# Performance work log

Measured on AMD Instinct MI355X. Metric: run time of the kernel, lower is better.

The kernel has to match this reference:

```python
import jax, jax.numpy as jnp
import numpy as np

B, T, IN, H = 512, 512, 1, 64


def _lstm_dir(x, w_ih, w_hh, b_ih, b_hh, reverse):
    """Single-direction LSTM over x:[B,T,D]. PyTorch gate order i,f,g,o."""
    # Precompute input contribution for all timesteps (one big GEMM).
    xg = jnp.einsum('btd,gd->btg', x, w_ih) + (b_ih + b_hh)  # [B,T,4H]
    if reverse:
        xg = xg[:, ::-1]
    Hh = w_hh.shape[1]
    w_hh_t = w_hh.T  # [H,4H]

    def step(carry, g_t):
        h, c = carry
        g = g_t + h @ w_hh_t  # [B,4H]
        i, f, gc, o = jnp.split(g, 4, axis=-1)
        c = jax.nn.sigmoid(f) * c + jax.nn.sigmoid(i) * jnp.tanh(gc)
        h = jax.nn.sigmoid(o) * jnp.tanh(c)
        return (h, c), h

    b = x.shape[0]
    init = (jnp.zeros((b, Hh), x.dtype), jnp.zeros((b, Hh), x.dtype))
    _, hs = jax.lax.scan(step, init, jnp.swapaxes(xg, 0, 1))  # hs:[T,B,H]
    hs = jnp.swapaxes(hs, 0, 1)  # [B,T,H]
    return hs[:, ::-1] if reverse else hs


def _bilstm_layer(x, wf, rf, bf, bf2, wr, rr, br, br2):
    fwd = _lstm_dir(x, wf, rf, bf, bf2, reverse=False)
    bwd = _lstm_dir(x, wr, rr, br, br2, reverse=True)
    return jnp.concatenate([fwd, bwd], axis=-1)  # [B,T,2H]


def setup_inputs() -> dict:
    key = jax.random.key(0)
    ks = jax.random.split(key, 20)
    s = 1.0 / np.sqrt(H)
    u = lambda k, shape: jax.random.uniform(k, shape, jnp.float32, -s, s)
    inp = {'x': jax.random.normal(ks[0], (B, T, IN), jnp.float32)}
    # layer 0 (input dim IN), layer 1 (input dim 2H), fwd and reverse dirs
    inp['w_ih_l0'] = u(ks[1], (4 * H, IN)); inp['w_hh_l0'] = u(ks[2], (4 * H, H))
    inp['b_ih_l0'] = u(ks[3], (4 * H,));   inp['b_hh_l0'] = u(ks[4], (4 * H,))
    inp['w_ih_l0r'] = u(ks[5], (4 * H, IN)); inp['w_hh_l0r'] = u(ks[6], (4 * H, H))
    inp['b_ih_l0r'] = u(ks[7], (4 * H,));    inp['b_hh_l0r'] = u(ks[8], (4 * H,))
    inp['w_ih_l1'] = u(ks[9], (4 * H, 2 * H)); inp['w_hh_l1'] = u(ks[10], (4 * H, H))
    inp['b_ih_l1'] = u(ks[11], (4 * H,));      inp['b_hh_l1'] = u(ks[12], (4 * H,))
    inp['w_ih_l1r'] = u(ks[13], (4 * H, 2 * H)); inp['w_hh_l1r'] = u(ks[14], (4 * H, H))
    inp['b_ih_l1r'] = u(ks[15], (4 * H,));       inp['b_hh_l1r'] = u(ks[16], (4 * H,))
    inp['fc_w'] = u(ks[17], (1, 2 * H)); inp['fc_b'] = u(ks[18], (1,))
    return inp


def reference(x, w_ih_l0, w_hh_l0, b_ih_l0, b_hh_l0,
              w_ih_l0r, w_hh_l0r, b_ih_l0r, b_hh_l0r,
              w_ih_l1, w_hh_l1, b_ih_l1, b_hh_l1,
              w_ih_l1r, w_hh_l1r, b_ih_l1r, b_hh_l1r,
              fc_w, fc_b):
    h0 = _bilstm_layer(x, w_ih_l0, w_hh_l0, b_ih_l0, b_hh_l0,
                       w_ih_l0r, w_hh_l0r, b_ih_l0r, b_hh_l0r)
    h1 = _bilstm_layer(h0, w_ih_l1, w_hh_l1, b_ih_l1, b_hh_l1,
                       w_ih_l1r, w_hh_l1r, b_ih_l1r, b_hh_l1r)
    last = h1[:, -1, :]  # [B,2H]
    return last @ fc_w.T + fc_b  # [B,1]
```

## Files before the change

### kernel.cpp

```cpp
#include <hip/hip_runtime.h>
#include <cstddef>
#include <cstdint>

#define Tn 512
#define Bn 512
#define Hn 64

__device__ __forceinline__ float rlane(float v, int lane) {
    return __uint_as_float((unsigned)__builtin_amdgcn_readlane((int)__float_as_uint(v), lane));
}
__device__ __forceinline__ float sigm(float x) { return 1.0f / (1.0f + __expf(-x)); }
__device__ __forceinline__ float tanhf_(float x) { return 1.0f - 2.0f / (1.0f + __expf(2.0f * x)); }

__global__ __launch_bounds__(64, 1) void k_lstm_l0(
    const float* __restrict__ x,
    const float* __restrict__ wih_f, const float* __restrict__ whh_f,
    const float* __restrict__ bih_f, const float* __restrict__ bhh_f,
    const float* __restrict__ wih_r, const float* __restrict__ whh_r,
    const float* __restrict__ bih_r, const float* __restrict__ bhh_r,
    float* __restrict__ h0)
{
    const int task = blockIdx.x;
    const int b = task >> 1;
    const int dir = task & 1;
    const int j = threadIdx.x;

    const float* __restrict__ wih = dir ? wih_r : wih_f;
    const float* __restrict__ whh = dir ? whh_r : whh_f;
    const float* __restrict__ bih = dir ? bih_r : bih_f;
    const float* __restrict__ bhh = dir ? bhh_r : bhh_f;

    __shared__ float xs[Tn];
    #pragma unroll
    for (int i = 0; i < Tn / 64; ++i) xs[i * 64 + j] = x[b * Tn + i * 64 + j];
    __syncthreads();

    float w[4][64];
    float wx[4], bias[4];
    #pragma unroll
    for (int g = 0; g < 4; ++g) {
        const int r = g * 64 + j;
        wx[g] = wih[r];
        bias[g] = bih[r] + bhh[r];
        #pragma unroll
        for (int k4 = 0; k4 < 16; ++k4) {
            const float4 v = *reinterpret_cast<const float4*>(&whh[r * 64 + k4 * 4]);
            w[g][k4 * 4 + 0] = v.x; w[g][k4 * 4 + 1] = v.y;
            w[g][k4 * 4 + 2] = v.z; w[g][k4 * 4 + 3] = v.w;
        }
    }

    float h = 0.0f, c = 0.0f;
    float* __restrict__ outp = h0 + (size_t)b * Tn * 128 + dir * 64 + j;

    for (int s = 0; s < Tn; ++s) {
        const int t = dir ? (Tn - 1 - s) : s;
        const float xt = xs[t];
        float a0 = fmaf(xt, wx[0], bias[0]);
        float a1 = fmaf(xt, wx[1], bias[1]);
        float a2 = fmaf(xt, wx[2], bias[2]);
        float a3 = fmaf(xt, wx[3], bias[3]);
        #pragma unroll
        for (int k = 0; k < 64; ++k) {
            const float hk = rlane(h, k);
            a0 = fmaf(hk, w[0][k], a0);
            a1 = fmaf(hk, w[1][k], a1);
            a2 = fmaf(hk, w[2][k], a2);
            a3 = fmaf(hk, w[3][k], a3);
        }
        c = sigm(a1) * c + sigm(a0) * tanhf_(a2);
        h = sigm(a3) * tanhf_(c);
        outp[(size_t)t * 128] = h;
    }
}

__global__ __launch_bounds__(256, 2) void k_lstm_l1f(
    const float* __restrict__ h0,
    const float* __restrict__ wih, const float* __restrict__ whh,
    const float* __restrict__ bih, const float* __restrict__ bhh,
    float* __restrict__ h1last)
{
    const int b = blockIdx.x;
    const int tid = threadIdx.x;
    const int wv = tid >> 6;
    const int j = tid & 63;

    float bias[4];
    #pragma unroll
    for (int g = 0; g < 4; ++g) {
        const int r = g * 64 + j;
        bias[g] = bih[r] + bhh[r];
    }

    float wt[4][48];
    if (wv == 0) {
        #pragma unroll
        for (int g = 0; g < 4; ++g) {
            const int r = g * 64 + j;
            #pragma unroll
            for (int kk = 0; kk < 48; ++kk) wt[g][kk] = wih[r * 128 + kk];
        }
    } else if (wv == 1) {
        #pragma unroll
        for (int g = 0; g < 4; ++g) {
            const int r = g * 64 + j;
            #pragma unroll
            for (int kk = 0; kk < 48; ++kk) wt[g][kk] = wih[r * 128 + 48 + kk];
        }
    } else if (wv == 2) {
        #pragma unroll
        for (int g = 0; g < 4; ++g) {
            const int r = g * 64 + j;
            #pragma unroll
            for (int kk = 0; kk < 48; ++kk)
                wt[g][kk] = (kk < 32) ? wih[r * 128 + 96 + kk] : whh[r * 64 + (kk - 32)];
        }
    } else {
        #pragma unroll
        for (int g = 0; g < 4; ++g) {
            const int r = g * 64 + j;
            #pragma unroll
            for (int kk = 0; kk < 48; ++kk) wt[g][kk] = whh[r * 64 + 16 + kk];
        }
    }

    const float* __restrict__ xrow = h0 + (size_t)b * Tn * 128;
    float x1a = xrow[j];
    float x1b = xrow[64 + j];
    float h = 0.0f, c = 0.0f;

    __shared__ float part[2][4][64][4];

    for (int t = 0; t < Tn; ++t) {
        float nx1a = 0.0f, nx1b = 0.0f;
        if (t + 1 < Tn) {
            nx1a = xrow[(t + 1) * 128 + j];
            nx1b = xrow[(t + 1) * 128 + 64 + j];
        }
        float a0 = 0.0f, a1 = 0.0f, a2 = 0.0f, a3 = 0.0f;
        if (wv == 0) {
            #pragma unroll
            for (int kk = 0; kk < 48; ++kk) {
                const float v = rlane(x1a, kk);
                a0 = fmaf(v, wt[0][kk], a0); a1 = fmaf(v, wt[1][kk], a1);
                a2 = fmaf(v, wt[2][kk], a2); a3 = fmaf(v, wt[3][kk], a3);
            }
        } else if (wv == 1) {
            #pragma unroll
            for (int kk = 0; kk < 48; ++kk) {
                const float v = (kk < 16) ? rlane(x1a, 48 + kk) : rlane(x1b, kk - 16);
                a0 = fmaf(v, wt[0][kk], a0); a1 = fmaf(v, wt[1][kk], a1);
                a2 = fmaf(v, wt[2][kk], a2); a3 = fmaf(v, wt[3][kk], a3);
            }
        } else if (wv == 2) {
            #pragma unroll
            for (int kk = 0; kk < 48; ++kk) {
                const float v = (kk < 32) ? rlane(x1b, 32 + kk) : rlane(h, kk - 32);
                a0 = fmaf(v, wt[0][kk], a0); a1 = fmaf(v, wt[1][kk], a1);
                a2 = fmaf(v, wt[2][kk], a2); a3 = fmaf(v, wt[3][kk], a3);
            }
        } else {
            #pragma unroll
            for (int kk = 0; kk < 48; ++kk) {
                const float v = rlane(h, 16 + kk);
                a0 = fmaf(v, wt[0][kk], a0); a1 = fmaf(v, wt[1][kk], a1);
                a2 = fmaf(v, wt[2][kk], a2); a3 = fmaf(v, wt[3][kk], a3);
            }
        }
        *reinterpret_cast<float4*>(&part[t & 1][wv][j][0]) = make_float4(a0, a1, a2, a3);
        __syncthreads();
        const float4 p0 = *reinterpret_cast<const float4*>(&part[t & 1][0][j][0]);
        const float4 p1 = *reinterpret_cast<const float4*>(&part[t & 1][1][j][0]);
        const float4 p2 = *reinterpret_cast<const float4*>(&part[t & 1][2][j][0]);
        const float4 p3 = *reinterpret_cast<const float4*>(&part[t & 1][3][j][0]);
        const float gi = bias[0] + p0.x + p1.x + p2.x + p3.x;
        const float gf = bias[1] + p0.y + p1.y + p2.y + p3.y;
        const float gg = bias[2] + p0.z + p1.z + p2.z + p3.z;
        const float go = bias[3] + p0.w + p1.w + p2.w + p3.w;
        c = sigm(gf) * c + sigm(gi) * tanhf_(gg);
        h = sigm(go) * tanhf_(c);
        x1a = nx1a; x1b = nx1b;
    }
    if (tid < 64) h1last[(size_t)b * 64 + j] = h;
}

__global__ __launch_bounds__(64, 1) void k_l1r_fc(
    const float* __restrict__ h0,
    const float* __restrict__ wihr,
    const float* __restrict__ bihr, const float* __restrict__ bhhr,
    const float* __restrict__ h1last,
    const float* __restrict__ fcw, const float* __restrict__ fcb,
    float* __restrict__ out)
{
    const int b = blockIdx.x;
    const int j = threadIdx.x;
    const float* __restrict__ xrow = h0 + ((size_t)b * Tn + (Tn - 1)) * 128;
    const float x1a = xrow[j];
    const float x1b = xrow[64 + j];
    float acc[4];
    #pragma unroll
    for (int g = 0; g < 4; ++g) {
        const int r = g * 64 + j;
        float a = bihr[r] + bhhr[r];
        const float* __restrict__ wr = wihr + (size_t)r * 128;
        #pragma unroll
        for (int d4 = 0; d4 < 16; ++d4) {
            const float4 w4 = *reinterpret_cast<const float4*>(&wr[d4 * 4]);
            a = fmaf(rlane(x1a, d4 * 4 + 0), w4.x, a);
            a = fmaf(rlane(x1a, d4 * 4 + 1), w4.y, a);
            a = fmaf(rlane(x1a, d4 * 4 + 2), w4.z, a);
            a = fmaf(rlane(x1a, d4 * 4 + 3), w4.w, a);
        }
        #pragma unroll
        for (int d4 = 0; d4 < 16; ++d4) {
            const float4 w4 = *reinterpret_cast<const float4*>(&wr[64 + d4 * 4]);
            a = fmaf(rlane(x1b, d4 * 4 + 0), w4.x, a);
            a = fmaf(rlane(x1b, d4 * 4 + 1), w4.y, a);
            a = fmaf(rlane(x1b, d4 * 4 + 2), w4.z, a);
            a = fmaf(rlane(x1b, d4 * 4 + 3), w4.w, a);
        }
        acc[g] = a;
    }
    const float cr = sigm(acc[0]) * tanhf_(acc[2]);
    const float hr = sigm(acc[3]) * tanhf_(cr);
    float v = h1last[(size_t)b * 64 + j] * fcw[j] + hr * fcw[64 + j];
    #pragma unroll
    for (int off = 32; off > 0; off >>= 1) v += __shfl_xor(v, off, 64);
    if (j == 0) out[b] = v + fcb[0];
}

extern "C" void kernel_launch(void* const* d_in, const int* in_sizes, int n_in,
                              void* d_out, int out_size, void* d_ws, size_t ws_size,
                              hipStream_t stream)
{
    const float* x       = (const float*)d_in[0];
    const float* wih_l0  = (const float*)d_in[1];
    const float* whh_l0  = (const float*)d_in[2];
    const float* bih_l0  = (const float*)d_in[3];
    const float* bhh_l0  = (const float*)d_in[4];
    const float* wih_l0r = (const float*)d_in[5];
    const float* whh_l0r = (const float*)d_in[6];
    const float* bih_l0r = (const float*)d_in[7];
    const float* bhh_l0r = (const float*)d_in[8];
    const float* wih_l1  = (const float*)d_in[9];
    const float* whh_l1  = (const float*)d_in[10];
    const float* bih_l1  = (const float*)d_in[11];
    const float* bhh_l1  = (const float*)d_in[12];
    const float* wih_l1r = (const float*)d_in[13];
    const float* whh_l1r = (const float*)d_in[14];
    const float* bih_l1r = (const float*)d_in[15];
    const float* bhh_l1r = (const float*)d_in[16];
    const float* fcw     = (const float*)d_in[17];
    const float* fcb     = (const float*)d_in[18];
    (void)whh_l1r; (void)in_sizes; (void)n_in; (void)out_size;

    float* h0     = (float*)d_ws;
    float* h1last = h0 + (size_t)Bn * Tn * 128;
    (void)ws_size;

    k_lstm_l0<<<dim3(Bn * 2), dim3(64), 0, stream>>>(
        x, wih_l0, whh_l0, bih_l0, bhh_l0,
        wih_l0r, whh_l0r, bih_l0r, bhh_l0r, h0);
    k_lstm_l1f<<<dim3(Bn), dim3(256), 0, stream>>>(
        h0, wih_l1, whh_l1, bih_l1, bhh_l1, h1last);
    k_l1r_fc<<<dim3(Bn), dim3(64), 0, stream>>>(
        h0, wih_l1r, bih_l1r, bhh_l1r, h1last, fcw, fcb, (float*)d_out);
}
```

Baseline: 1.207 ms.

## Split LSTM recurrence K-dimension across more waves in both layer kernels

Layer 0 now runs both directions of a batch row in one 256-thread block, with each direction's 64-wide hidden dot product split across two waves whose partial gate sums are combined through shared memory. Layer 1 forward uses six waves of 32 K-columns each, so every wave does a uniform 32-step readlane/FMA loop instead of four waves doing 48. Two waves redundantly apply the gate nonlinearities and feed h back as their next input. This shortens the serial per-step dependency chain and lowers register pressure, at the cost of an extra barrier per step in layer 0 and more waves competing for each CU.

```diff
diff --git a/kernel.cpp b/kernel.cpp
--- a/kernel.cpp
+++ b/kernel.cpp
@@ -4,7 +4,6 @@
 
 #define Tn 512
 #define Bn 512
-#define Hn 64
 
 __device__ __forceinline__ float rlane(float v, int lane) {
     return __uint_as_float((unsigned)__builtin_amdgcn_readlane((int)__float_as_uint(v), lane));
@@ -12,7 +11,9 @@
 __device__ __forceinline__ float sigm(float x) { return 1.0f / (1.0f + __expf(-x)); }
 __device__ __forceinline__ float tanhf_(float x) { return 1.0f - 2.0f / (1.0f + __expf(2.0f * x)); }
 
-__global__ __launch_bounds__(64, 1) void k_lstm_l0(
+#define BAR_LGKM() asm volatile("s_waitcnt lgkmcnt(0)\n\ts_barrier" ::: "memory")
+
+__global__ __launch_bounds__(256, 2) void k_lstm_l0(
     const float* __restrict__ x,
     const float* __restrict__ wih_f, const float* __restrict__ whh_f,
     const float* __restrict__ bih_f, const float* __restrict__ bhh_f,
@@ -20,168 +21,148 @@
     const float* __restrict__ bih_r, const float* __restrict__ bhh_r,
     float* __restrict__ h0)
 {
-    const int task = blockIdx.x;
-    const int b = task >> 1;
-    const int dir = task & 1;
-    const int j = threadIdx.x;
+    const int b   = blockIdx.x;
+    const int tid = threadIdx.x;
+    const int wv  = tid >> 6;
+    const int dir = wv >> 1;
+    const int kh  = wv & 1;
+    const int j   = tid & 63;
+    const int klo = kh * 32;
 
     const float* __restrict__ wih = dir ? wih_r : wih_f;
     const float* __restrict__ whh = dir ? whh_r : whh_f;
     const float* __restrict__ bih = dir ? bih_r : bih_f;
     const float* __restrict__ bhh = dir ? bhh_r : bhh_f;
 
-    __shared__ float xs[Tn];
-    #pragma unroll
-    for (int i = 0; i < Tn / 64; ++i) xs[i * 64 + j] = x[b * Tn + i * 64 + j];
-    __syncthreads();
-
-    float w[4][64];
+    __shared__ float  xs[Tn];
+    __shared__ float4 part[2][4][64];
+
+    #pragma unroll
+    for (int i = 0; i < Tn / 256; ++i) xs[i * 256 + tid] = x[b * Tn + i * 256 + tid];
+
+    float wt[4][32];
     float wx[4], bias[4];
     #pragma unroll
     for (int g = 0; g < 4; ++g) {
         const int r = g * 64 + j;
-        wx[g] = wih[r];
+        wx[g]   = wih[r];
         bias[g] = bih[r] + bhh[r];
-        #pragma unroll
-        for (int k4 = 0; k4 < 16; ++k4) {
-            const float4 v = *reinterpret_cast<const float4*>(&whh[r * 64 + k4 * 4]);
-            w[g][k4 * 4 + 0] = v.x; w[g][k4 * 4 + 1] = v.y;
-            w[g][k4 * 4 + 2] = v.z; w[g][k4 * 4 + 3] = v.w;
-        }
-    }
+        const float* __restrict__ ws = whh + (size_t)r * 64 + klo;
+        #pragma unroll
+        for (int k4 = 0; k4 < 8; ++k4) {
+            const float4 w4 = *reinterpret_cast<const float4*>(ws + k4 * 4);
+            wt[g][k4 * 4 + 0] = w4.x; wt[g][k4 * 4 + 1] = w4.y;
+            wt[g][k4 * 4 + 2] = w4.z; wt[g][k4 * 4 + 3] = w4.w;
+        }
+    }
+    __syncthreads();
 
     float h = 0.0f, c = 0.0f;
     float* __restrict__ outp = h0 + (size_t)b * Tn * 128 + dir * 64 + j;
 
     for (int s = 0; s < Tn; ++s) {
-        const int t = dir ? (Tn - 1 - s) : s;
+        const int t  = dir ? (Tn - 1 - s) : s;
+        const int bf = s & 1;
         const float xt = xs[t];
-        float a0 = fmaf(xt, wx[0], bias[0]);
-        float a1 = fmaf(xt, wx[1], bias[1]);
-        float a2 = fmaf(xt, wx[2], bias[2]);
-        float a3 = fmaf(xt, wx[3], bias[3]);
-        #pragma unroll
-        for (int k = 0; k < 64; ++k) {
-            const float hk = rlane(h, k);
-            a0 = fmaf(hk, w[0][k], a0);
-            a1 = fmaf(hk, w[1][k], a1);
-            a2 = fmaf(hk, w[2][k], a2);
-            a3 = fmaf(hk, w[3][k], a3);
-        }
-        c = sigm(a1) * c + sigm(a0) * tanhf_(a2);
-        h = sigm(a3) * tanhf_(c);
-        outp[(size_t)t * 128] = h;
-    }
-}
-
-__global__ __launch_bounds__(256, 2) void k_lstm_l1f(
+
+        float a0 = 0.0f, a1 = 0.0f, a2 = 0.0f, a3 = 0.0f;
+        #pragma unroll
+        for (int kk = 0; kk < 32; ++kk) {
+            const float hk = rlane(h, klo + kk);
+            a0 = fmaf(hk, wt[0][kk], a0);
+            a1 = fmaf(hk, wt[1][kk], a1);
+            a2 = fmaf(hk, wt[2][kk], a2);
+            a3 = fmaf(hk, wt[3][kk], a3);
+        }
+        part[bf][wv][j] = make_float4(a0, a1, a2, a3);
+        BAR_LGKM();
+        const float4 pA = part[bf][dir * 2 + 0][j];
+        const float4 pB = part[bf][dir * 2 + 1][j];
+        const float gi = fmaf(xt, wx[0], bias[0]) + pA.x + pB.x;
+        const float gf = fmaf(xt, wx[1], bias[1]) + pA.y + pB.y;
+        const float gg = fmaf(xt, wx[2], bias[2]) + pA.z + pB.z;
+        const float go = fmaf(xt, wx[3], bias[3]) + pA.w + pB.w;
+        c = sigm(gf) * c + sigm(gi) * tanhf_(gg);
+        h = sigm(go) * tanhf_(c);
+        if (kh == 0) outp[(size_t)t * 128] = h;
+    }
+}
+
+__global__ __launch_bounds__(384, 3) void k_lstm_l1f(
     const float* __restrict__ h0,
     const float* __restrict__ wih, const float* __restrict__ whh,
     const float* __restrict__ bih, const float* __restrict__ bhh,
     float* __restrict__ h1last)
 {
-    const int b = blockIdx.x;
+    const int b   = blockIdx.x;
     const int tid = threadIdx.x;
-    const int wv = tid >> 6;
-    const int j = tid & 63;
-
+    const int wv  = tid / 64;
+    const int j   = tid & 63;
+    const int lb  = (wv & 1) * 32;
+    const int kbase = wv * 32;
+
+    __shared__ float4 part[2][6][64];
+
+    float wt[4][32];
     float bias[4];
     #pragma unroll
     for (int g = 0; g < 4; ++g) {
         const int r = g * 64 + j;
         bias[g] = bih[r] + bhh[r];
-    }
-
-    float wt[4][48];
-    if (wv == 0) {
-        #pragma unroll
-        for (int g = 0; g < 4; ++g) {
-            const int r = g * 64 + j;
-            #pragma unroll
-            for (int kk = 0; kk < 48; ++kk) wt[g][kk] = wih[r * 128 + kk];
-        }
-    } else if (wv == 1) {
-        #pragma unroll
-        for (int g = 0; g < 4; ++g) {
-            const int r = g * 64 + j;
-            #pragma unroll
-            for (int kk = 0; kk < 48; ++kk) wt[g][kk] = wih[r * 128 + 48 + kk];
-        }
-    } else if (wv == 2) {
-        #pragma unroll
-        for (int g = 0; g < 4; ++g) {
-            const int r = g * 64 + j;
-            #pragma unroll
-            for (int kk = 0; kk < 48; ++kk)
-                wt[g][kk] = (kk < 32) ? wih[r * 128 + 96 + kk] : whh[r * 64 + (kk - 32)];
-        }
-    } else {
-        #pragma unroll
-        for (int g = 0; g < 4; ++g) {
-            const int r = g * 64 + j;
-            #pragma unroll
-            for (int kk = 0; kk < 48; ++kk) wt[g][kk] = whh[r * 64 + 16 + kk];
+        const float* __restrict__ ws = (kbase < 128)
+            ? (wih + (size_t)r * 128 + kbase)
+            : (whh + (size_t)r * 64 + (kbase - 128));
+        #pragma unroll
+        for (int k4 = 0; k4 < 8; ++k4) {
+            const float4 w4 = *reinterpret_cast<const float4*>(ws + k4 * 4);
+            wt[g][k4 * 4 + 0] = w4.x; wt[g][k4 * 4 + 1] = w4.y;
+            wt[g][k4 * 4 + 2] = w4.z; wt[g][k4 * 4 + 3] = w4.w;
         }
     }
 
     const float* __restrict__ xrow = h0 + (size_t)b * Tn * 128;
-    float x1a = xrow[j];
-    float x1b = xrow[64 + j];
+    const int goff = (wv >> 1) * 64;
+
+    float src = 0.0f;
+    if (wv < 4) src = xrow[goff + j];
     float h = 0.0f, c = 0.0f;
 
-    __shared__ float part[2][4][64][4];
-
     for (int t = 0; t < Tn; ++t) {
-        float nx1a = 0.0f, nx1b = 0.0f;
-        if (t + 1 < Tn) {
-            nx1a = xrow[(t + 1) * 128 + j];
-            nx1b = xrow[(t + 1) * 128 + 64 + j];
+        const int bf = t & 1;
+        float nsrc = src;
+        if (wv < 4) {
+            const int tn = (t + 1 < Tn) ? (t + 1) : t;
+            nsrc = xrow[(size_t)tn * 128 + goff + j];
         }
         float a0 = 0.0f, a1 = 0.0f, a2 = 0.0f, a3 = 0.0f;
-        if (wv == 0) {
-            #pragma unroll
-            for (int kk = 0; kk < 48; ++kk) {
-                const float v = rlane(x1a, kk);
-                a0 = fmaf(v, wt[0][kk], a0); a1 = fmaf(v, wt[1][kk], a1);
-                a2 = fmaf(v, wt[2][kk], a2); a3 = fmaf(v, wt[3][kk], a3);
-            }
-        } else if (wv == 1) {
-            #pragma unroll
-            for (int kk = 0; kk < 48; ++kk) {
-                const float v = (kk < 16) ? rlane(x1a, 48 + kk) : rlane(x1b, kk - 16);
-                a0 = fmaf(v, wt[0][kk], a0); a1 = fmaf(v, wt[1][kk], a1);
-                a2 = fmaf(v, wt[2][kk], a2); a3 = fmaf(v, wt[3][kk], a3);
-            }
-        } else if (wv == 2) {
-            #pragma unroll
-            for (int kk = 0; kk < 48; ++kk) {
-                const float v = (kk < 32) ? rlane(x1b, 32 + kk) : rlane(h, kk - 32);
-                a0 = fmaf(v, wt[0][kk], a0); a1 = fmaf(v, wt[1][kk], a1);
-                a2 = fmaf(v, wt[2][kk], a2); a3 = fmaf(v, wt[3][kk], a3);
-            }
-        } else {
-            #pragma unroll
-            for (int kk = 0; kk < 48; ++kk) {
-                const float v = rlane(h, 16 + kk);
-                a0 = fmaf(v, wt[0][kk], a0); a1 = fmaf(v, wt[1][kk], a1);
-                a2 = fmaf(v, wt[2][kk], a2); a3 = fmaf(v, wt[3][kk], a3);
-            }
-        }
-        *reinterpret_cast<float4*>(&part[t & 1][wv][j][0]) = make_float4(a0, a1, a2, a3);
-        __syncthreads();
-        const float4 p0 = *reinterpret_cast<const float4*>(&part[t & 1][0][j][0]);
-        const float4 p1 = *reinterpret_cast<const float4*>(&part[t & 1][1][j][0]);
-        const float4 p2 = *reinterpret_cast<const float4*>(&part[t & 1][2][j][0]);
-        const float4 p3 = *reinterpret_cast<const float4*>(&part[t & 1][3][j][0]);
-        const float gi = bias[0] + p0.x + p1.x + p2.x + p3.x;
-        const float gf = bias[1] + p0.y + p1.y + p2.y + p3.y;
-        const float gg = bias[2] + p0.z + p1.z + p2.z + p3.z;
-        const float go = bias[3] + p0.w + p1.w + p2.w + p3.w;
-        c = sigm(gf) * c + sigm(gi) * tanhf_(gg);
-        h = sigm(go) * tanhf_(c);
-        x1a = nx1a; x1b = nx1b;
-    }
-    if (tid < 64) h1last[(size_t)b * 64 + j] = h;
+        #pragma unroll
+        for (int kk = 0; kk < 32; ++kk) {
+            const float v = rlane(src, lb + kk);
+            a0 = fmaf(v, wt[0][kk], a0);
+            a1 = fmaf(v, wt[1][kk], a1);
+            a2 = fmaf(v, wt[2][kk], a2);
+            a3 = fmaf(v, wt[3][kk], a3);
+        }
+        part[bf][wv][j] = make_float4(a0, a1, a2, a3);
+        BAR_LGKM();
+        if (wv >= 4) {
+            const float4 q0 = part[bf][0][j];
+            const float4 q1 = part[bf][1][j];
+            const float4 q2 = part[bf][2][j];
+            const float4 q3 = part[bf][3][j];
+            const float4 q4 = part[bf][4][j];
+            const float4 q5 = part[bf][5][j];
+            const float gi = bias[0] + q0.x + q1.x + q2.x + q3.x + q4.x + q5.x;
+            const float gf = bias[1] + q0.y + q1.y + q2.y + q3.y + q4.y + q5.y;
+            const float gg = bias[2] + q0.z + q1.z + q2.z + q3.z + q4.z + q5.z;
+            const float go = bias[3] + q0.w + q1.w + q2.w + q3.w + q4.w + q5.w;
+            c = sigm(gf) * c + sigm(gi) * tanhf_(gg);
+            h = sigm(go) * tanhf_(c);
+        }
+        src = nsrc;
+        if (wv >= 4) src = h;
+    }
+    if (wv == 4) h1last[(size_t)b * 64 + j] = h;
 }
 
 __global__ __launch_bounds__(64, 1) void k_l1r_fc(
@@ -258,10 +239,10 @@
     float* h1last = h0 + (size_t)Bn * Tn * 128;
     (void)ws_size;
 
-    k_lstm_l0<<<dim3(Bn * 2), dim3(64), 0, stream>>>(
+    k_lstm_l0<<<dim3(Bn), dim3(256), 0, stream>>>(
         x, wih_l0, whh_l0, bih_l0, bhh_l0,
         wih_l0r, whh_l0r, bih_l0r, bhh_l0r, h0);
-    k_lstm_l1f<<<dim3(Bn), dim3(256), 0, stream>>>(
+    k_lstm_l1f<<<dim3(Bn), dim3(384), 0, stream>>>(
         h0, wih_l1, whh_l1, bih_l1, bhh_l1, h1last);
     k_l1r_fc<<<dim3(Bn), dim3(64), 0, stream>>>(
         h0, wih_l1r, bih_l1r, bhh_l1r, h1last, fcw, fcb, (float*)d_out);
```

New measurement: 2.988 ms. +147.5%, slower.
